# Kernel optimization log

Hardware: AMD Instinct MI355X
Metric: run time of the kernel (lower is better)

The kernel has to match this reference:

```python
import jax, jax.numpy as jnp
import numpy as np

KERNEL_SIZE = 5
PAD = (KERNEL_SIZE - 1) // 2  # ZeroPad2d(2)
MID = PAD
# all 24 kernel offsets except the center (documented intent of the module)
OFFSETS = [(i, j) for i in range(KERNEL_SIZE) for j in range(KERNEL_SIZE)
           if not (i == MID and j == MID)]


def setup_inputs() -> dict:
    key = jax.random.key(0)
    k1, k2, k3 = jax.random.split(key, 3)
    B, C, H, Wd = 16, 1, 512, 512
    OUT = 32
    x = jax.random.normal(k1, (B, C, H, Wd), dtype=jnp.float32)
    # 1x1 conv weight [out_ch, in_ch=24] (squeezed from [out,24,1,1]) and bias
    W = jax.random.normal(k2, (OUT, 24), dtype=jnp.float32) * 0.1
    b = jax.random.normal(k3, (OUT,), dtype=jnp.float32) * 0.1
    return {"x": x, "W": W, "b": b}


def reference(x, W, b):
    B, C, H, Wd = x.shape  # C == 1
    xp = jnp.pad(x, ((0, 0), (0, 0), (PAD, PAD), (PAD, PAD)))
    # shift-subtract: 24 neighbor differences, concatenated on channel dim
    chans = jnp.concatenate(
        [xp[:, :, i:H + i, j:Wd + j] - x for (i, j) in OFFSETS], axis=1
    )  # [B, 24, H, W]
    # 1x1 conv = per-pixel channel mix
    out = jnp.einsum('bchw,oc->bohw', chans, W) + b[None, :, None, None]
    return out
```

## Files before the change

kernel.cpp:

```cpp
#include <hip/hip_runtime.h>


#define H_DIM 512
#define W_DIM 512
#define BATCH 16
#define OUTC 32

#define TILE_W 256
#define TILE_H 4
#define BLOCK_X 64
#define BLOCK_Y 4
#define HALO_W (TILE_W + 4)
#define LDS_W  (TILE_W + 8)
#define LDS_H  (TILE_H + 4)

__global__ __launch_bounds__(64) void pc_prep(const float* __restrict__ W,
                                              float* __restrict__ K) {
    int o = threadIdx.x;
    if (o < OUTC) {
        float s = 0.f;
        #pragma unroll
        for (int c = 0; c < 24; ++c) s += W[o * 24 + c];
        #pragma unroll
        for (int t = 0; t < 25; ++t) {
            float v = (t == 12) ? -s : W[o * 24 + (t < 12 ? t : t - 1)];
            K[o * 25 + t] = v;
        }
    }
}

__global__ __launch_bounds__(256) void pc_conv(const float* __restrict__ x,
                                               const float* __restrict__ K,
                                               const float* __restrict__ bias,
                                               float* __restrict__ out) {
    __shared__ float lds[LDS_H * LDS_W];

    const int b  = blockIdx.z;
    const int h0 = blockIdx.y * TILE_H;
    const int w0 = blockIdx.x * TILE_W;
    const int tx = threadIdx.x;
    const int ty = threadIdx.y;
    const int tid = ty * BLOCK_X + tx;

    const float* xb = x + (size_t)b * H_DIM * W_DIM;

    for (int idx = tid; idx < LDS_H * HALO_W; idx += BLOCK_X * BLOCK_Y) {
        int r = idx / HALO_W;
        int c = idx - r * HALO_W;
        int gh = h0 - 2 + r;
        int gw = w0 - 2 + c;
        float v = 0.f;
        if ((unsigned)gh < (unsigned)H_DIM && (unsigned)gw < (unsigned)W_DIM)
            v = xb[gh * W_DIM + gw];
        lds[r * LDS_W + c] = v;
    }
    __syncthreads();

    float nb[5][8];
    #pragma unroll
    for (int r = 0; r < 5; ++r) {
        const float4* p = (const float4*)&lds[(ty + r) * LDS_W + 4 * tx];
        float4 a = p[0];
        float4 c = p[1];
        nb[r][0] = a.x; nb[r][1] = a.y; nb[r][2] = a.z; nb[r][3] = a.w;
        nb[r][4] = c.x; nb[r][5] = c.y; nb[r][6] = c.z; nb[r][7] = c.w;
    }

    const int h = h0 + ty;
    const int w = w0 + 4 * tx;
    float* op = out + (size_t)b * OUTC * H_DIM * W_DIM + (size_t)h * W_DIM + w;

    #pragma unroll 1
    for (int o = 0; o < OUTC; ++o) {
        const float* kr = K + o * 25;
        float bb = bias[o];
        float acc0 = bb, acc1 = bb, acc2 = bb, acc3 = bb;
        #pragma unroll
        for (int ki = 0; ki < 5; ++ki) {
            #pragma unroll
            for (int kj = 0; kj < 5; ++kj) {
                float k = kr[ki * 5 + kj];
                acc0 += k * nb[ki][kj + 0];
                acc1 += k * nb[ki][kj + 1];
                acc2 += k * nb[ki][kj + 2];
                acc3 += k * nb[ki][kj + 3];
            }
        }
        *(float4*)op = make_float4(acc0, acc1, acc2, acc3);
        op += H_DIM * W_DIM;
    }
}

extern "C" void kernel_launch(void* const* d_in, const int* in_sizes, int n_in,
                              void* d_out, int out_size, void* d_ws, size_t ws_size,
                              hipStream_t stream) {
    const float* x    = (const float*)d_in[0];
    const float* W    = (const float*)d_in[1];
    const float* bias = (const float*)d_in[2];
    float* out = (float*)d_out;
    float* K   = (float*)d_ws;

    pc_prep<<<1, 64, 0, stream>>>(W, K);

    dim3 grid(W_DIM / TILE_W, H_DIM / TILE_H, BATCH);
    dim3 block(BLOCK_X, BLOCK_Y, 1);
    pc_conv<<<grid, block, 0, stream>>>(x, K, bias, out);
}
```

Baseline: 547.7 us.

## Compute two output rows per thread and rotate channel order per block

Each thread now produces two adjacent output rows, reusing a 6-row register window of neighbors, with TILE_H doubled to 8 so there are half as many blocks. The bias is folded into the prepared K table (stride 26), and the 26 weights per channel are loaded once into registers for both rows. Output-channel iteration is rotated by blockIdx.y, which looks aimed at spreading concurrent writes across different memory regions. The output is about 512 MB of writes, so the kernel is likely write-bandwidth bound and the compute reuse may matter little. Register pressure also goes up.

```diff
diff --git a/kernel.cpp b/kernel.cpp
--- a/kernel.cpp
+++ b/kernel.cpp
@@ -5,9 +5,10 @@
 #define W_DIM 512
 #define BATCH 16
 #define OUTC 32
+#define KROW 26
 
 #define TILE_W 256
-#define TILE_H 4
+#define TILE_H 8
 #define BLOCK_X 64
 #define BLOCK_Y 4
 #define HALO_W (TILE_W + 4)
@@ -15,6 +16,7 @@
 #define LDS_H  (TILE_H + 4)
 
 __global__ __launch_bounds__(64) void pc_prep(const float* __restrict__ W,
+                                              const float* __restrict__ bias,
                                               float* __restrict__ K) {
     int o = threadIdx.x;
     if (o < OUTC) {
@@ -24,14 +26,14 @@
         #pragma unroll
         for (int t = 0; t < 25; ++t) {
             float v = (t == 12) ? -s : W[o * 24 + (t < 12 ? t : t - 1)];
-            K[o * 25 + t] = v;
+            K[o * KROW + t] = v;
         }
+        K[o * KROW + 25] = bias[o];
     }
 }
 
 __global__ __launch_bounds__(256) void pc_conv(const float* __restrict__ x,
                                                const float* __restrict__ K,
-                                               const float* __restrict__ bias,
                                                float* __restrict__ out) {
     __shared__ float lds[LDS_H * LDS_W];
 
@@ -40,54 +42,70 @@
     const int w0 = blockIdx.x * TILE_W;
     const int tx = threadIdx.x;
     const int ty = threadIdx.y;
-    const int tid = ty * BLOCK_X + tx;
 
     const float* xb = x + (size_t)b * H_DIM * W_DIM;
 
-    for (int idx = tid; idx < LDS_H * HALO_W; idx += BLOCK_X * BLOCK_Y) {
-        int r = idx / HALO_W;
-        int c = idx - r * HALO_W;
-        int gh = h0 - 2 + r;
-        int gw = w0 - 2 + c;
-        float v = 0.f;
-        if ((unsigned)gh < (unsigned)H_DIM && (unsigned)gw < (unsigned)W_DIM)
-            v = xb[gh * W_DIM + gw];
-        lds[r * LDS_W + c] = v;
+    for (int r = ty; r < LDS_H; r += BLOCK_Y) {
+        const int gh = h0 - 2 + r;
+        #pragma unroll
+        for (int c0 = 0; c0 < HALO_W; c0 += BLOCK_X) {
+            const int c = c0 + tx;
+            if (c < HALO_W) {
+                const int gw = w0 - 2 + c;
+                float v = 0.f;
+                if ((unsigned)gh < (unsigned)H_DIM && (unsigned)gw < (unsigned)W_DIM)
+                    v = xb[gh * W_DIM + gw];
+                lds[r * LDS_W + c] = v;
+            }
+        }
     }
     __syncthreads();
 
-    float nb[5][8];
+    float nb[6][8];
     #pragma unroll
-    for (int r = 0; r < 5; ++r) {
-        const float4* p = (const float4*)&lds[(ty + r) * LDS_W + 4 * tx];
+    for (int r = 0; r < 6; ++r) {
+        const float4* p = (const float4*)&lds[(2 * ty + r) * LDS_W + 4 * tx];
         float4 a = p[0];
         float4 c = p[1];
         nb[r][0] = a.x; nb[r][1] = a.y; nb[r][2] = a.z; nb[r][3] = a.w;
         nb[r][4] = c.x; nb[r][5] = c.y; nb[r][6] = c.z; nb[r][7] = c.w;
     }
 
-    const int h = h0 + ty;
+    const int h = h0 + 2 * ty;
     const int w = w0 + 4 * tx;
-    float* op = out + (size_t)b * OUTC * H_DIM * W_DIM + (size_t)h * W_DIM + w;
+    const int rot = blockIdx.y & 31;
+    float* obase = out + (size_t)b * OUTC * H_DIM * W_DIM
+                       + (size_t)h * W_DIM + w;
 
-    #pragma unroll 1
-    for (int o = 0; o < OUTC; ++o) {
-        const float* kr = K + o * 25;
-        float bb = bias[o];
-        float acc0 = bb, acc1 = bb, acc2 = bb, acc3 = bb;
+    #pragma unroll 2
+    for (int oo = 0; oo < OUTC; ++oo) {
+        const int o = (oo + rot) & 31;
+        const float* kr = K + o * KROW;
+        float kk[26];
+        #pragma unroll
+        for (int t = 0; t < 26; ++t) kk[t] = kr[t];
+
+        const float bb = kk[25];
+        float a0 = bb, a1 = bb, a2 = bb, a3 = bb;
+        float b0 = bb, b1 = bb, b2 = bb, b3 = bb;
         #pragma unroll
         for (int ki = 0; ki < 5; ++ki) {
             #pragma unroll
             for (int kj = 0; kj < 5; ++kj) {
-                float k = kr[ki * 5 + kj];
-                acc0 += k * nb[ki][kj + 0];
-                acc1 += k * nb[ki][kj + 1];
-                acc2 += k * nb[ki][kj + 2];
-                acc3 += k * nb[ki][kj + 3];
+                const float k = kk[ki * 5 + kj];
+                a0 += k * nb[ki][kj + 0];
+                a1 += k * nb[ki][kj + 1];
+                a2 += k * nb[ki][kj + 2];
+                a3 += k * nb[ki][kj + 3];
+                b0 += k * nb[ki + 1][kj + 0];
+                b1 += k * nb[ki + 1][kj + 1];
+                b2 += k * nb[ki + 1][kj + 2];
+                b3 += k * nb[ki + 1][kj + 3];
             }
         }
-        *(float4*)op = make_float4(acc0, acc1, acc2, acc3);
-        op += H_DIM * W_DIM;
+        float* op = obase + (size_t)o * (H_DIM * W_DIM);
+        *(float4*)op            = make_float4(a0, a1, a2, a3);
+        *(float4*)(op + W_DIM)  = make_float4(b0, b1, b2, b3);
     }
 }
 
@@ -100,9 +118,9 @@
     float* out = (float*)d_out;
     float* K   = (float*)d_ws;
 
-    pc_prep<<<1, 64, 0, stream>>>(W, K);
+    pc_prep<<<1, 64, 0, stream>>>(W, bias, K);
 
     dim3 grid(W_DIM / TILE_W, H_DIM / TILE_H, BATCH);
     dim3 block(BLOCK_X, BLOCK_Y, 1);
-    pc_conv<<<grid, block, 0, stream>>>(x, K, bias, out);
+    pc_conv<<<grid, block, 0, stream>>>(x, K, out);
 }
```

After: 587.6 us. 7.3% more time.

## Parallelize output channels across grid blocks instead of looping per block

Applied to the files above, without the earlier changes.

Each block now computes a single output channel, with the channel index folded into blockIdx.z, so the grid grows 32x and the per-block 32-channel loop is gone. The bias is packed into the prepared filter buffer at a padded row stride. The halo load is restructured into row/column loops without a divide. The cost is that every block reloads the input tile into LDS, giving 32x redundant input reads and LDS fills in exchange for more parallelism and shorter blocks.

```diff
diff --git a/kernel.cpp b/kernel.cpp
--- a/kernel.cpp
+++ b/kernel.cpp
@@ -5,6 +5,7 @@
 #define W_DIM 512
 #define BATCH 16
 #define OUTC 32
+#define KROW 26
 
 #define TILE_W 256
 #define TILE_H 4
@@ -15,6 +16,7 @@
 #define LDS_H  (TILE_H + 4)
 
 __global__ __launch_bounds__(64) void pc_prep(const float* __restrict__ W,
+                                              const float* __restrict__ bias,
                                               float* __restrict__ K) {
     int o = threadIdx.x;
     if (o < OUTC) {
@@ -24,35 +26,40 @@
         #pragma unroll
         for (int t = 0; t < 25; ++t) {
             float v = (t == 12) ? -s : W[o * 24 + (t < 12 ? t : t - 1)];
-            K[o * 25 + t] = v;
+            K[o * KROW + t] = v;
         }
+        K[o * KROW + 25] = bias[o];
     }
 }
 
 __global__ __launch_bounds__(256) void pc_conv(const float* __restrict__ x,
                                                const float* __restrict__ K,
-                                               const float* __restrict__ bias,
                                                float* __restrict__ out) {
     __shared__ float lds[LDS_H * LDS_W];
 
-    const int b  = blockIdx.z;
+    const int z  = blockIdx.z;
+    const int b  = z >> 5;
+    const int o  = z & 31;
     const int h0 = blockIdx.y * TILE_H;
     const int w0 = blockIdx.x * TILE_W;
     const int tx = threadIdx.x;
     const int ty = threadIdx.y;
-    const int tid = ty * BLOCK_X + tx;
 
     const float* xb = x + (size_t)b * H_DIM * W_DIM;
 
-    for (int idx = tid; idx < LDS_H * HALO_W; idx += BLOCK_X * BLOCK_Y) {
-        int r = idx / HALO_W;
-        int c = idx - r * HALO_W;
-        int gh = h0 - 2 + r;
-        int gw = w0 - 2 + c;
-        float v = 0.f;
-        if ((unsigned)gh < (unsigned)H_DIM && (unsigned)gw < (unsigned)W_DIM)
-            v = xb[gh * W_DIM + gw];
-        lds[r * LDS_W + c] = v;
+    for (int r = ty; r < LDS_H; r += BLOCK_Y) {
+        const int gh = h0 - 2 + r;
+        #pragma unroll
+        for (int c0 = 0; c0 < HALO_W; c0 += BLOCK_X) {
+            const int c = c0 + tx;
+            if (c < HALO_W) {
+                const int gw = w0 - 2 + c;
+                float v = 0.f;
+                if ((unsigned)gh < (unsigned)H_DIM && (unsigned)gw < (unsigned)W_DIM)
+                    v = xb[gh * W_DIM + gw];
+                lds[r * LDS_W + c] = v;
+            }
+        }
     }
     __syncthreads();
 
@@ -68,27 +75,25 @@
 
     const int h = h0 + ty;
     const int w = w0 + 4 * tx;
-    float* op = out + (size_t)b * OUTC * H_DIM * W_DIM + (size_t)h * W_DIM + w;
 
-    #pragma unroll 1
-    for (int o = 0; o < OUTC; ++o) {
-        const float* kr = K + o * 25;
-        float bb = bias[o];
-        float acc0 = bb, acc1 = bb, acc2 = bb, acc3 = bb;
+    const float* kr = K + o * KROW;
+    const float bb = kr[25];
+    float acc0 = bb, acc1 = bb, acc2 = bb, acc3 = bb;
+    #pragma unroll
+    for (int ki = 0; ki < 5; ++ki) {
         #pragma unroll
-        for (int ki = 0; ki < 5; ++ki) {
-            #pragma unroll
-            for (int kj = 0; kj < 5; ++kj) {
-                float k = kr[ki * 5 + kj];
-                acc0 += k * nb[ki][kj + 0];
-                acc1 += k * nb[ki][kj + 1];
-                acc2 += k * nb[ki][kj + 2];
-                acc3 += k * nb[ki][kj + 3];
-            }
+        for (int kj = 0; kj < 5; ++kj) {
+            const float k = kr[ki * 5 + kj];
+            acc0 += k * nb[ki][kj + 0];
+            acc1 += k * nb[ki][kj + 1];
+            acc2 += k * nb[ki][kj + 2];
+            acc3 += k * nb[ki][kj + 3];
         }
-        *(float4*)op = make_float4(acc0, acc1, acc2, acc3);
-        op += H_DIM * W_DIM;
     }
+
+    float* op = out + (size_t)(b * OUTC + o) * (H_DIM * W_DIM)
+                    + (size_t)h * W_DIM + w;
+    *(float4*)op = make_float4(acc0, acc1, acc2, acc3);
 }
 
 extern "C" void kernel_launch(void* const* d_in, const int* in_sizes, int n_in,
@@ -100,9 +105,9 @@
     float* out = (float*)d_out;
     float* K   = (float*)d_ws;
 
-    pc_prep<<<1, 64, 0, stream>>>(W, K);
+    pc_prep<<<1, 64, 0, stream>>>(W, bias, K);
 
-    dim3 grid(W_DIM / TILE_W, H_DIM / TILE_H, BATCH);
+    dim3 grid(W_DIM / TILE_W, H_DIM / TILE_H, BATCH * OUTC);
     dim3 block(BLOCK_X, BLOCK_Y, 1);
-    pc_conv<<<grid, block, 0, stream>>>(x, K, bias, out);
+    pc_conv<<<grid, block, 0, stream>>>(x, K, out);
 }
```

Result: slower. 710.7 us (+29.8%).
